# Kernel tuning notes

Measured on AMD Instinct MI355X. Metric: run time of the kernel, lower is better.

Reference implementation:

```python
import jax, jax.numpy as jnp
import numpy as np

NUM_HEADS = 4
KEY_DIM = 64
D_MODEL = 256
OUTPUT_DIM = 256


def setup_inputs() -> dict:
    key = jax.random.key(0)
    ks = jax.random.split(key, 11)
    B, T, D = 16, 1024, D_MODEL
    HD = NUM_HEADS * KEY_DIM
    s = 0.02
    return {
        "query": jax.random.normal(ks[0], (B, T, D), jnp.float32),
        "key": jax.random.normal(ks[1], (B, T, D), jnp.float32),
        "value": jax.random.normal(ks[2], (B, T, D), jnp.float32),
        "Wq": jax.random.normal(ks[3], (D, HD), jnp.float32) * s,
        "bq": jnp.zeros((HD,), jnp.float32),
        "Wk": jax.random.normal(ks[4], (D, HD), jnp.float32) * s,
        "bk": jnp.zeros((HD,), jnp.float32),
        "Wv": jax.random.normal(ks[5], (D, KEY_DIM), jnp.float32) * s,
        "bv": jnp.zeros((KEY_DIM,), jnp.float32),
        "Wo": jax.random.normal(ks[6], (HD, OUTPUT_DIM), jnp.float32) * s,
        "bo": jnp.zeros((OUTPUT_DIM,), jnp.float32),
    }


def reference(query, key, value, Wq, bq, Wk, bk, Wv, bv, Wo, bo):
    B, Tq, _ = query.shape
    Tk = key.shape[1]
    H, Dk = NUM_HEADS, KEY_DIM
    # projections
    q = (query @ Wq + bq).reshape(B, Tq, H, Dk)  # [B,Tq,H,Dk]
    k = (key @ Wk + bk).reshape(B, Tk, H, Dk)    # [B,Tk,H,Dk]
    v = value @ Wv + bv                           # [B,Tk,Dk] shared across heads
    scale = jnp.asarray(Dk, q.dtype) ** -0.5
    # scores [B,H,Tq,Tk]
    score = jnp.einsum("bqhd,bkhd->bhqk", q, k) * scale
    attn = jax.nn.softmax(score, axis=-1)
    # broadcast-V attention: [B,H,Tq,Tk] x [B,Tk,Dk] -> [B,H,Tq,Dk]
    out = jnp.einsum("bhqk,bkd->bhqd", attn, v)
    out = out.transpose(0, 2, 1, 3).reshape(B, Tq, H * Dk)
    return out @ Wo + bo
```

## Files before the change

kernel.cpp:

```cpp
#include <hip/hip_runtime.h>
#include <hip/hip_bf16.h>


typedef __attribute__((ext_vector_type(8))) short short8;
typedef __attribute__((ext_vector_type(4))) float f32x4;
typedef __attribute__((ext_vector_type(16))) float f32x16;

__device__ __forceinline__ short f2bf(float x) {
    return __builtin_bit_cast(short, __float2bfloat16(x));
}

__device__ __forceinline__ float exp2_fast(float x) {
#if __has_builtin(__builtin_amdgcn_exp2f)
    return __builtin_amdgcn_exp2f(x);
#else
    float r; asm("v_exp_f32 %0, %1" : "=v"(r) : "v"(x)); return r;
#endif
}

__device__ __forceinline__ f32x4 mfma16(short8 a, short8 b, f32x4 c) {
    return __builtin_amdgcn_mfma_f32_16x16x32_bf16(a, b, c, 0, 0, 0);
}
__device__ __forceinline__ f32x16 mfma32(short8 a, short8 b, f32x16 c) {
    return __builtin_amdgcn_mfma_f32_32x32x16_bf16(a, b, c, 0, 0, 0);
}

__device__ __forceinline__ int cvtpk(float lo, float hi) {
    int r; asm("v_cvt_pk_bf16_f32 %0, %1, %2" : "=v"(r) : "v"(lo), "v"(hi));
    return r;
}
__device__ __forceinline__ void swap32(int& a, int& b) {
    asm("v_permlane32_swap_b32 %0, %1" : "+v"(a), "+v"(b));
}

__device__ __forceinline__ short8 half_frag(const f32x16& s, int base) {
    int d0 = cvtpk(s[base + 0], s[base + 1]);
    int d1 = cvtpk(s[base + 2], s[base + 3]);
    int d2 = cvtpk(s[base + 4], s[base + 5]);
    int d3 = cvtpk(s[base + 6], s[base + 7]);
    swap32(d0, d2);
    swap32(d1, d3);
    int4 v = { d0, d1, d2, d3 };
    return __builtin_bit_cast(short8, v);
}

__device__ __forceinline__ float sum16(const f32x16& e) {
    return (((e[0] + e[1]) + (e[2] + e[3])) + ((e[4] + e[5]) + (e[6] + e[7])))
         + (((e[8] + e[9]) + (e[10] + e[11])) + ((e[12] + e[13]) + (e[14] + e[15])));
}

#define QSCALE 0.18033688011112042f

__global__ void prep_weights(const float* __restrict__ Wq, const float* __restrict__ Wk,
                             const float* __restrict__ Wv, const float* __restrict__ Wo,
                             short* __restrict__ WqtF, short* __restrict__ WktF,
                             short* __restrict__ WvtF, short* __restrict__ WotF) {
    int tid = blockIdx.x * 256 + threadIdx.x;
    int k = tid >> 8, n = tid & 255;
    int off = ((n >> 6) << 14) + (((n >> 4) & 3) << 12) + ((k >> 5) << 9)
            + (((k >> 3) & 3) << 7) + ((n & 15) << 3) + (k & 7);
    WqtF[off] = f2bf(Wq[k * 256 + n] * QSCALE);
    WktF[off] = f2bf(Wk[k * 256 + n]);
    int offo = ((n >> 5) << 13) + ((k >> 4) << 9) + (((k & 15) >> 3) << 8)
             + ((n & 31) << 3) + (k & 7);
    WotF[offo] = f2bf(Wo[k * 256 + n]);
    if (n < 64) {
        int offv = ((n >> 4) << 12) + ((k >> 5) << 9) + (((k >> 3) & 3) << 7)
                 + ((n & 15) << 3) + (k & 7);
        WvtF[offv] = f2bf(Wv[k * 64 + n]);
    }
}

__global__ __launch_bounds__(256) void proj_all(
        const float* __restrict__ query, const float* __restrict__ key_,
        const float* __restrict__ value,
        const short* __restrict__ WqtF, const short* __restrict__ WktF,
        const short* __restrict__ WvtF,
        const float* __restrict__ bq, const float* __restrict__ bk,
        const float* __restrict__ bv,
        short* __restrict__ qf, short* __restrict__ kf, short* __restrict__ vf) {
    __shared__ short At[8192];
    const int tid = threadIdx.x;
    const int lane = tid & 63, wave = tid >> 6;
    const int u = lane >> 4, r16 = lane & 15;
    const int m0 = blockIdx.x * 32;
    const int task = blockIdx.y;

    const float* A = task == 0 ? query : (task == 1 ? key_ : value);

    #pragma unroll
    for (int j = 0; j < 4; ++j) {
        int p8 = j * 8 + ((wave >> 1) << 2) + u;
        int row = ((wave & 1) << 4) + r16;
        const float* src = A + (m0 + row) * 256 + p8 * 8;
        float4 a0 = *(const float4*)src;
        float4 a1 = *(const float4*)(src + 4);
        short8 w;
        w[0] = f2bf(a0.x); w[1] = f2bf(a0.y); w[2] = f2bf(a0.z); w[3] = f2bf(a0.w);
        w[4] = f2bf(a1.x); w[5] = f2bf(a1.y); w[6] = f2bf(a1.z); w[7] = f2bf(a1.w);
        int dst = ((p8 >> 2) << 10) + ((wave & 1) << 9) + ((p8 & 3) << 7) + (r16 << 3);
        *(short8*)&At[dst] = w;
    }

    const int b = m0 >> 10, t32 = (m0 >> 5) & 31;

    if (task < 2) {
        const short* WtF = task == 0 ? WqtF : WktF;
        const float* bias = task == 0 ? bq : bk;
        const float bscale = task == 0 ? QSCALE : 1.0f;
        short* outF = task == 0 ? qf : kf;
        const short* wb = WtF + (wave << 14);

        short8 bf8[4];
        #pragma unroll
        for (int g = 0; g < 4; ++g) bf8[g] = *(const short8*)&wb[(g << 12) + lane * 8];
        __syncthreads();

        f32x4 acc[2][4] = {};
        #pragma unroll
        for (int kk = 0; kk < 8; ++kk) {
            short8 af[2], nb[4];
            #pragma unroll
            for (int f = 0; f < 2; ++f) af[f] = *(const short8*)&At[(kk << 10) + (f << 9) + lane * 8];
            if (kk < 7) {
                #pragma unroll
                for (int g = 0; g < 4; ++g) nb[g] = *(const short8*)&wb[(g << 12) + ((kk + 1) << 9) + lane * 8];
            }
            #pragma unroll
            for (int f = 0; f < 2; ++f)
                #pragma unroll
                for (int g = 0; g < 4; ++g)
                    acc[f][g] = mfma16(af[f], bf8[g], acc[f][g]);
            #pragma unroll
            for (int g = 0; g < 4; ++g) bf8[g] = nb[g];
        }

        float bvv[4];
        #pragma unroll
        for (int g = 0; g < 4; ++g) bvv[g] = bias[(wave << 6) + 16 * g + r16] * bscale;
        short* ob = outF + ((((b << 2) + wave) << 5) + t32) * 2048;
        #pragma unroll
        for (int f = 0; f < 2; ++f)
            #pragma unroll
            for (int g = 0; g < 4; ++g)
                #pragma unroll
                for (int rr = 0; rr < 4; ++rr)
                    ob[(g << 9) + ((r16 >> 3) << 8) + (16 * f + 4 * u + rr) * 8 + (r16 & 7)]
                        = f2bf(acc[f][g][rr] + bvv[g]);
    } else {
        const int fr = wave >> 1;
        short8 bf8[2];
        #pragma unroll
        for (int z = 0; z < 2; ++z) {
            int dg = ((wave & 1) << 1) + z;
            bf8[z] = *(const short8*)&WvtF[(dg << 12) + lane * 8];
        }
        __syncthreads();

        f32x4 acc[2] = {};
        #pragma unroll
        for (int kk = 0; kk < 8; ++kk) {
            short8 af = *(const short8*)&At[(kk << 10) + (fr << 9) + lane * 8];
            short8 nb[2];
            if (kk < 7) {
                #pragma unroll
                for (int z = 0; z < 2; ++z) {
                    int dg = ((wave & 1) << 1) + z;
                    nb[z] = *(const short8*)&WvtF[(dg << 12) + ((kk + 1) << 9) + lane * 8];
                }
            }
            #pragma unroll
            for (int z = 0; z < 2; ++z) acc[z] = mfma16(af, bf8[z], acc[z]);
            bf8[0] = nb[0]; bf8[1] = nb[1];
        }

        short* ob = vf + ((b << 5) + t32) * 2048;
        #pragma unroll
        for (int z = 0; z < 2; ++z) {
            int dg = ((wave & 1) << 1) + z;
            float bvv = bv[16 * dg + r16];
            #pragma unroll
            for (int rr = 0; rr < 4; ++rr) {
                int tl = 4 * u + rr;
                ob[((dg >> 1) << 10) + (fr << 9) + ((tl >> 3) << 8)
                   + ((16 * (dg & 1) + r16) << 3) + (tl & 7)]
                    = f2bf(acc[z][rr] + bvv);
            }
        }
    }
}

__global__ __launch_bounds__(512, 2) void attn_og(const short* __restrict__ qF,
        const short* __restrict__ kF, const short* __restrict__ vF,
        const short* __restrict__ WoF, const float* __restrict__ bo,
        float* __restrict__ outp) {
    __shared__ float ocm[16384];
    __shared__ float lcm[512];
    __shared__ short At[16384];
    const int tid = threadIdx.x;
    const int lane = tid & 63, wave = tid >> 6;
    const int h = wave >> 1, kvh = wave & 1;
    const int u2 = lane >> 5, n31 = lane & 31;

    const int L = (blockIdx.x & 7) * 32 + (blockIdx.x >> 3);
    const int b = L >> 4, qt = L & 15;

    const short* qb = qF + ((((b << 2) + h) << 5) + (qt << 1)) * 2048;
    short8 Q0[4], Q1[4];
    #pragma unroll
    for (int c = 0; c < 4; ++c) {
        Q0[c] = *(const short8*)&qb[(c << 9) + lane * 8];
        Q1[c] = *(const short8*)&qb[2048 + (c << 9) + lane * 8];
    }

    const short* kb = kF + ((((b << 2) + h) << 5) + (kvh << 4)) * 2048;
    const short* vb = vF + (((b << 5) + (kvh << 4))) * 2048;

    short8 kfr[4], vfr[4];
    #pragma unroll
    for (int c = 0; c < 4; ++c) {
        kfr[c] = *(const short8*)&kb[(c << 9) + lane * 8];
        vfr[c] = *(const short8*)&vb[(c << 9) + lane * 8];
    }

    f32x16 aO00 = {}, aO01 = {}, aO10 = {}, aO11 = {};
    float l0 = 0.f, l1 = 0.f;

    for (int i = 0; i < 16; ++i) {
        short8 nk[4], nv[4];
        if (i < 15) {
            const short* kn = kb + (i + 1) * 2048;
            const short* vn = vb + (i + 1) * 2048;
            #pragma unroll
            for (int c = 0; c < 4; ++c) {
                nk[c] = *(const short8*)&kn[(c << 9) + lane * 8];
                nv[c] = *(const short8*)&vn[(c << 9) + lane * 8];
            }
        }

        f32x16 S0 = {}, S1 = {};
        S0 = mfma32(kfr[0], Q0[0], S0); S1 = mfma32(kfr[0], Q1[0], S1);
        S0 = mfma32(kfr[1], Q0[1], S0); S1 = mfma32(kfr[1], Q1[1], S1);
        S0 = mfma32(kfr[2], Q0[2], S0); S1 = mfma32(kfr[2], Q1[2], S1);
        S0 = mfma32(kfr[3], Q0[3], S0); S1 = mfma32(kfr[3], Q1[3], S1);

        #pragma unroll
        for (int j = 0; j < 16; ++j) S0[j] = exp2_fast(S0[j]);
        #pragma unroll
        for (int j = 0; j < 16; ++j) S1[j] = exp2_fast(S1[j]);
        l0 += sum16(S0);
        l1 += sum16(S1);

        short8 p00 = half_frag(S0, 0), p01 = half_frag(S0, 8);
        short8 p10 = half_frag(S1, 0), p11 = half_frag(S1, 8);

        aO00 = mfma32(vfr[0], p00, aO00); aO00 = mfma32(vfr[1], p01, aO00);
        aO10 = mfma32(vfr[2], p00, aO10); aO10 = mfma32(vfr[3], p01, aO10);
        aO01 = mfma32(vfr[0], p10, aO01); aO01 = mfma32(vfr[1], p11, aO01);
        aO11 = mfma32(vfr[2], p10, aO11); aO11 = mfma32(vfr[3], p11, aO11);

        #pragma unroll
        for (int c = 0; c < 4; ++c) { kfr[c] = nk[c]; vfr[c] = nv[c]; }
    }

    l0 += __shfl_xor(l0, 32);
    l1 += __shfl_xor(l1, 32);

    float4* ocm4 = (float4*)ocm;
    if (kvh == 1) {
        #pragma unroll
        for (int j4 = 0; j4 < 4; ++j4) {
            float4 w0 = { aO00[4 * j4], aO00[4 * j4 + 1], aO00[4 * j4 + 2], aO00[4 * j4 + 3] };
            float4 w1 = { aO10[4 * j4], aO10[4 * j4 + 1], aO10[4 * j4 + 2], aO10[4 * j4 + 3] };
            float4 w2 = { aO01[4 * j4], aO01[4 * j4 + 1], aO01[4 * j4 + 2], aO01[4 * j4 + 3] };
            float4 w3 = { aO11[4 * j4], aO11[4 * j4 + 1], aO11[4 * j4 + 2], aO11[4 * j4 + 3] };
            ocm4[(((h << 2) + 0) * 4 + j4) * 64 + lane] = w0;
            ocm4[(((h << 2) + 1) * 4 + j4) * 64 + lane] = w1;
            ocm4[(((h << 2) + 2) * 4 + j4) * 64 + lane] = w2;
            ocm4[(((h << 2) + 3) * 4 + j4) * 64 + lane] = w3;
        }
        lcm[(h << 1) * 64 + lane] = l0;
        lcm[((h << 1) + 1) * 64 + lane] = l1;
    }
    __syncthreads();

    if (kvh == 0) {
        #pragma unroll
        for (int j4 = 0; j4 < 4; ++j4) {
            float4 r0 = ocm4[(((h << 2) + 0) * 4 + j4) * 64 + lane];
            float4 r1 = ocm4[(((h << 2) + 1) * 4 + j4) * 64 + lane];
            float4 r2 = ocm4[(((h << 2) + 2) * 4 + j4) * 64 + lane];
            float4 r3 = ocm4[(((h << 2) + 3) * 4 + j4) * 64 + lane];
            #pragma unroll
            for (int e = 0; e < 4; ++e) {
                aO00[4 * j4 + e] += ((const float*)&r0)[e];
                aO10[4 * j4 + e] += ((const float*)&r1)[e];
                aO01[4 * j4 + e] += ((const float*)&r2)[e];
                aO11[4 * j4 + e] += ((const float*)&r3)[e];
            }
        }
        float li0 = 1.0f / (l0 + lcm[(h << 1) * 64 + lane]);
        float li1 = 1.0f / (l1 + lcm[((h << 1) + 1) * 64 + lane]);

        #pragma unroll
        for (int j = 0; j < 16; ++j) {
            aO00[j] *= li0; aO10[j] *= li0;
            aO01[j] *= li1; aO11[j] *= li1;
        }

        short8 a00 = half_frag(aO00, 0), a01 = half_frag(aO00, 8);
        short8 a10 = half_frag(aO10, 0), a11 = half_frag(aO10, 8);
        short8 b00 = half_frag(aO01, 0), b01 = half_frag(aO01, 8);
        short8 b10 = half_frag(aO11, 0), b11 = half_frag(aO11, 8);
        *(short8*)&At[(((h << 2) + 0) << 9) + lane * 8] = a00;
        *(short8*)&At[(((h << 2) + 1) << 9) + lane * 8] = a01;
        *(short8*)&At[(((h << 2) + 2) << 9) + lane * 8] = a10;
        *(short8*)&At[(((h << 2) + 3) << 9) + lane * 8] = a11;
        *(short8*)&At[8192 + (((h << 2) + 0) << 9) + lane * 8] = b00;
        *(short8*)&At[8192 + (((h << 2) + 1) << 9) + lane * 8] = b01;
        *(short8*)&At[8192 + (((h << 2) + 2) << 9) + lane * 8] = b10;
        *(short8*)&At[8192 + (((h << 2) + 3) << 9) + lane * 8] = b11;
    }
    __syncthreads();

    const int qtile = wave >> 2, np = wave & 3;
    const short* at = &At[qtile << 13];
    const short* wo0 = WoF + (2 * np) * 8192;
    const short* wo1 = wo0 + 8192;
    f32x16 acc20 = {}, acc21 = {};
    #pragma unroll
    for (int kc = 0; kc < 16; ++kc) {
        short8 a = *(const short8*)&at[(kc << 9) + lane * 8];
        short8 w0 = *(const short8*)&wo0[(kc << 9) + lane * 8];
        short8 w1 = *(const short8*)&wo1[(kc << 9) + lane * 8];
        acc20 = mfma32(a, w0, acc20);
        acc21 = mfma32(a, w1, acc21);
    }

    const int m0 = (L << 6) + (qtile << 5);
    {
        float bv0 = bo[(2 * np) * 32 + n31];
        float bv1 = bo[(2 * np + 1) * 32 + n31];
        #pragma unroll
        for (int r = 0; r < 16; ++r) {
            int q = (r & 3) + 8 * (r >> 2) + 4 * u2;
            outp[(m0 + q) * 256 + (2 * np) * 32 + n31] = acc20[r] + bv0;
            outp[(m0 + q) * 256 + (2 * np + 1) * 32 + n31] = acc21[r] + bv1;
        }
    }
}

extern "C" void kernel_launch(void* const* d_in, const int* in_sizes, int n_in,
                              void* d_out, int out_size, void* d_ws, size_t ws_size,
                              hipStream_t stream) {
    (void)in_sizes; (void)n_in; (void)out_size; (void)ws_size;
    const float* query = (const float*)d_in[0];
    const float* key_  = (const float*)d_in[1];
    const float* value = (const float*)d_in[2];
    const float* Wq = (const float*)d_in[3];
    const float* bq = (const float*)d_in[4];
    const float* Wk = (const float*)d_in[5];
    const float* bk = (const float*)d_in[6];
    const float* Wv = (const float*)d_in[7];
    const float* bv = (const float*)d_in[8];
    const float* Wo = (const float*)d_in[9];
    const float* bo = (const float*)d_in[10];
    float* outp = (float*)d_out;

    short* wsp  = (short*)d_ws;
    short* WqtF = wsp;
    short* WktF = wsp + 65536;
    short* WotF = wsp + 131072;
    short* WvtF = wsp + 196608;
    short* qf   = wsp + 212992;
    short* kf   = wsp + 4407296;
    short* vf   = wsp + 8601600;

    hipLaunchKernelGGL(prep_weights, dim3(256), dim3(256), 0, stream,
                       Wq, Wk, Wv, Wo, WqtF, WktF, WvtF, WotF);
    hipLaunchKernelGGL(proj_all, dim3(512, 3), dim3(256), 0, stream,
                       query, key_, value, WqtF, WktF, WvtF, bq, bk, bv, qf, kf, vf);
    hipLaunchKernelGGL(attn_og, dim3(256), dim3(512), 0, stream,
                       qf, kf, vf, WotF, bo, outp);
}
```

Baseline: 52.84 us.

## Software-pipeline QK scores one tile ahead of softmax and PV in attention loop

Restructures the key-tile loop so the QK^T MFMA for tile i+1 is issued while exp2/sum/pack of tile i runs, then the PV MFMAs for tile i. K is prefetched two tiles ahead and V one tile ahead. The aim is to overlap transcendental and conversion VALU work with matrix-core work and hide load latency. It costs more live registers (an extra score accumulator pair) and issues some redundant clamped loads at the tail.

```diff
diff --git a/kernel.cpp b/kernel.cpp
--- a/kernel.cpp
+++ b/kernel.cpp
@@ -216,51 +216,59 @@
     const short* kb = kF + ((((b << 2) + h) << 5) + (kvh << 4)) * 2048;
     const short* vb = vF + (((b << 5) + (kvh << 4))) * 2048;
 
-    short8 kfr[4], vfr[4];
+    short8 kx[4], vc[4];
     #pragma unroll
     for (int c = 0; c < 4; ++c) {
-        kfr[c] = *(const short8*)&kb[(c << 9) + lane * 8];
-        vfr[c] = *(const short8*)&vb[(c << 9) + lane * 8];
-    }
+        kx[c] = *(const short8*)&kb[(c << 9) + lane * 8];
+        vc[c] = *(const short8*)&vb[(c << 9) + lane * 8];
+    }
+
+    f32x16 S0p = {}, S1p = {};
+    S0p = mfma32(kx[0], Q0[0], S0p); S1p = mfma32(kx[0], Q1[0], S1p);
+    S0p = mfma32(kx[1], Q0[1], S0p); S1p = mfma32(kx[1], Q1[1], S1p);
+    S0p = mfma32(kx[2], Q0[2], S0p); S1p = mfma32(kx[2], Q1[2], S1p);
+    S0p = mfma32(kx[3], Q0[3], S0p); S1p = mfma32(kx[3], Q1[3], S1p);
+
+    #pragma unroll
+    for (int c = 0; c < 4; ++c)
+        kx[c] = *(const short8*)&kb[2048 + (c << 9) + lane * 8];
 
     f32x16 aO00 = {}, aO01 = {}, aO10 = {}, aO11 = {};
     float l0 = 0.f, l1 = 0.f;
 
     for (int i = 0; i < 16; ++i) {
-        short8 nk[4], nv[4];
-        if (i < 15) {
-            const short* kn = kb + (i + 1) * 2048;
-            const short* vn = vb + (i + 1) * 2048;
+        #pragma unroll
+        for (int j = 0; j < 16; ++j) S0p[j] = exp2_fast(S0p[j]);
+        #pragma unroll
+        for (int j = 0; j < 16; ++j) S1p[j] = exp2_fast(S1p[j]);
+        l0 += sum16(S0p);
+        l1 += sum16(S1p);
+        short8 p00 = half_frag(S0p, 0), p01 = half_frag(S0p, 8);
+        short8 p10 = half_frag(S1p, 0), p11 = half_frag(S1p, 8);
+
+        f32x16 T0 = {}, T1 = {};
+        T0 = mfma32(kx[0], Q0[0], T0); T1 = mfma32(kx[0], Q1[0], T1);
+        T0 = mfma32(kx[1], Q0[1], T0); T1 = mfma32(kx[1], Q1[1], T1);
+        T0 = mfma32(kx[2], Q0[2], T0); T1 = mfma32(kx[2], Q1[2], T1);
+        T0 = mfma32(kx[3], Q0[3], T0); T1 = mfma32(kx[3], Q1[3], T1);
+        S0p = T0; S1p = T1;
+
+        aO00 = mfma32(vc[0], p00, aO00); aO00 = mfma32(vc[1], p01, aO00);
+        aO10 = mfma32(vc[2], p00, aO10); aO10 = mfma32(vc[3], p01, aO10);
+        aO01 = mfma32(vc[0], p10, aO01); aO01 = mfma32(vc[1], p11, aO01);
+        aO11 = mfma32(vc[2], p10, aO11); aO11 = mfma32(vc[3], p11, aO11);
+
+        {
+            int iv = i + 1 < 16 ? i + 1 : 15;
+            int ik = i + 2 < 16 ? i + 2 : 15;
+            const short* vn = vb + iv * 2048;
+            const short* kn = kb + ik * 2048;
             #pragma unroll
             for (int c = 0; c < 4; ++c) {
-                nk[c] = *(const short8*)&kn[(c << 9) + lane * 8];
-                nv[c] = *(const short8*)&vn[(c << 9) + lane * 8];
-            }
-        }
-
-        f32x16 S0 = {}, S1 = {};
-        S0 = mfma32(kfr[0], Q0[0], S0); S1 = mfma32(kfr[0], Q1[0], S1);
-        S0 = mfma32(kfr[1], Q0[1], S0); S1 = mfma32(kfr[1], Q1[1], S1);
-        S0 = mfma32(kfr[2], Q0[2], S0); S1 = mfma32(kfr[2], Q1[2], S1);
-        S0 = mfma32(kfr[3], Q0[3], S0); S1 = mfma32(kfr[3], Q1[3], S1);
-
-        #pragma unroll
-        for (int j = 0; j < 16; ++j) S0[j] = exp2_fast(S0[j]);
-        #pragma unroll
-        for (int j = 0; j < 16; ++j) S1[j] = exp2_fast(S1[j]);
-        l0 += sum16(S0);
-        l1 += sum16(S1);
-
-        short8 p00 = half_frag(S0, 0), p01 = half_frag(S0, 8);
-        short8 p10 = half_frag(S1, 0), p11 = half_frag(S1, 8);
-
-        aO00 = mfma32(vfr[0], p00, aO00); aO00 = mfma32(vfr[1], p01, aO00);
-        aO10 = mfma32(vfr[2], p00, aO10); aO10 = mfma32(vfr[3], p01, aO10);
-        aO01 = mfma32(vfr[0], p10, aO01); aO01 = mfma32(vfr[1], p11, aO01);
-        aO11 = mfma32(vfr[2], p10, aO11); aO11 = mfma32(vfr[3], p11, aO11);
-
-        #pragma unroll
-        for (int c = 0; c < 4; ++c) { kfr[c] = nk[c]; vfr[c] = nv[c]; }
+                vc[c] = *(const short8*)&vn[(c << 9) + lane * 8];
+                kx[c] = *(const short8*)&kn[(c << 9) + lane * 8];
+            }
+        }
     }
 
     l0 += __shfl_xor(l0, 32);
```

New measurement: 53.36 us. No clear change (+1.0%).
